# Kernel tuning notes

Measured on AMD Instinct MI355X. Metric: run time of the kernel, lower is better.

Reference implementation:

```python
import jax, jax.numpy as jnp
import numpy as np

B, C, T, D, LI = 512, 6, 77, 512, 193  # batch, noun chunks, context len, embed dim, image tokens
VOCAB = 49408


def setup_inputs() -> dict:
    key = jax.random.key(0)
    k1, k2, k3, k4 = jax.random.split(key, 4)
    return {
        "image_features": jax.random.normal(k1, (B, LI, D), dtype=jnp.float32),
        "text_features": jax.random.normal(k2, (B, T, D), dtype=jnp.float32),
        "logit_scale": jnp.ones((1,), dtype=jnp.float32) * 4.6052,
        "captions": jax.random.randint(k3, (B, T), 0, VOCAB, dtype=jnp.int32),
        "noun_chunk_mask": jax.random.randint(k4, (B, C, T), 0, 2, dtype=jnp.int32),
    }


def reference(image_features, text_features, logit_scale, captions, noun_chunk_mask):
    # global image feature: CLS token
    global_image = image_features[:, 0, :]                      # (B, D)
    # global text feature: token at argmax(captions) (EOT position in CLIP)
    eot = jnp.argmax(captions, axis=-1)                         # (B,)
    global_text = text_features[jnp.arange(text_features.shape[0]), eot]  # (B, D)
    # local text features: per-noun-chunk masked mean over the 77 token positions.
    # Original: (repeat_cap * mask).mean(dim=2) == (mask @ text_features) / 77.
    m = noun_chunk_mask.astype(text_features.dtype)             # (B, C, T) 0/1
    local_text = jnp.einsum('bct,btd->bcd', m, text_features) / float(T)  # (B, C, D)
    return (global_text, global_image, local_text, logit_scale)
```

## Files before the change

### kernel.cpp

```cpp
#include <hip/hip_runtime.h>

#define BB 512
#define CC 6
#define TT 77
#define DD 512
#define LIMG 193

__global__ __launch_bounds__(512) void clip_fused(
    const float* __restrict__ img,
    const float* __restrict__ txt,
    const float* __restrict__ ls,
    const int* __restrict__ cap,
    const int* __restrict__ mask,
    float* __restrict__ out)
{
    const int b   = blockIdx.x;
    const int tid = threadIdx.x;
    const int col = tid & 127;
    const int q   = tid >> 7;

    __shared__ float m[CC * TT];
    __shared__ int   wred[8];
    __shared__ float4 part[4][CC][128];

    const int* mrow = mask + (size_t)b * (CC * TT);
    for (int i = tid; i < CC * TT; i += 512) m[i] = (float)mrow[i];

    const int* crow = cap + (size_t)b * TT;
    int key = -1;
    if (tid < TT) key = (crow[tid] << 8) | (255 - tid);
    #pragma unroll
    for (int off = 32; off; off >>= 1) key = max(key, __shfl_down(key, off));
    if ((tid & 63) == 0) wred[tid >> 6] = key;
    __syncthreads();

    int kmax = wred[0];
    #pragma unroll
    for (int w = 1; w < 8; w++) kmax = max(kmax, wred[w]);
    const int eot = 255 - (kmax & 255);

    const float4* trow = (const float4*)(txt + (size_t)b * (TT * DD));

    if (q == 0) {
        float4 g = trow[(size_t)eot * 128 + col];
        ((float4*)out)[(size_t)b * 128 + col] = g;
    } else if (q == 1) {
        const float4* irow = (const float4*)(img + (size_t)b * (LIMG * DD));
        ((float4*)(out + (size_t)BB * DD))[(size_t)b * 128 + col] = irow[col];
    }

    float4 acc[CC];
    #pragma unroll
    for (int c = 0; c < CC; c++) acc[c] = make_float4(0.f, 0.f, 0.f, 0.f);

    #pragma unroll 5
    for (int t = q; t < TT; t += 4) {
        float4 v = trow[(size_t)t * 128 + col];
        #pragma unroll
        for (int c = 0; c < CC; c++) {
            float w = m[c * TT + t];
            acc[c].x += w * v.x;
            acc[c].y += w * v.y;
            acc[c].z += w * v.z;
            acc[c].w += w * v.w;
        }
    }
    #pragma unroll
    for (int c = 0; c < CC; c++) part[q][c][col] = acc[c];
    __syncthreads();

    float4* out_lt = (float4*)(out + 2 * (size_t)BB * DD);
    const float inv = 1.0f / (float)TT;
    for (int i = tid; i < CC * 128; i += 512) {
        int c  = i >> 7;
        int cc = i & 127;
        float4 s0 = part[0][c][cc];
        float4 s1 = part[1][c][cc];
        float4 s2 = part[2][c][cc];
        float4 s3 = part[3][c][cc];
        float4 r;
        r.x = (s0.x + s1.x + s2.x + s3.x) * inv;
        r.y = (s0.y + s1.y + s2.y + s3.y) * inv;
        r.z = (s0.z + s1.z + s2.z + s3.z) * inv;
        r.w = (s0.w + s1.w + s2.w + s3.w) * inv;
        out_lt[((size_t)b * CC + c) * 128 + cc] = r;
    }

    if (b == 0 && tid == 0)
        out[(size_t)2 * BB * DD + (size_t)BB * CC * DD] = ls[0];
}

extern "C" void kernel_launch(void* const* d_in, const int* in_sizes, int n_in,
                              void* d_out, int out_size, void* d_ws, size_t ws_size,
                              hipStream_t stream) {
    const float* img  = (const float*)d_in[0];
    const float* txt  = (const float*)d_in[1];
    const float* ls   = (const float*)d_in[2];
    const int*   cap  = (const int*)d_in[3];
    const int*   mask = (const int*)d_in[4];
    float* out = (float*)d_out;

    clip_fused<<<dim3(BB), dim3(512), 0, stream>>>(img, txt, ls, cap, mask, out);
}
```

Measured before the change: 286.6 us.

## Split each batch across two blocks and reduce partial sums with wave shuffles

Launches two blocks per batch, each covering half of the feature columns. Within a block, 8 lanes each take a strided subset of token positions, and their partial sums are combined with shuffle-down instead of a shared-memory partial buffer plus a second barrier. The mask is stored transposed and padded to 8 so one vector load fetches all chunk weights for a token, and launch bounds request higher occupancy. The trade-off is that adjacent lanes now read different token rows, which breaks per-row coalescing into 8-element groups, and the mask is loaded twice per batch.

```diff
diff --git a/kernel.cpp b/kernel.cpp
--- a/kernel.cpp
+++ b/kernel.cpp
@@ -6,7 +6,7 @@
 #define DD 512
 #define LIMG 193
 
-__global__ __launch_bounds__(512) void clip_fused(
+__global__ __launch_bounds__(512, 8) void clip_fused(
     const float* __restrict__ img,
     const float* __restrict__ txt,
     const float* __restrict__ ls,
@@ -14,79 +14,95 @@
     const int* __restrict__ mask,
     float* __restrict__ out)
 {
-    const int b   = blockIdx.x;
-    const int tid = threadIdx.x;
-    const int col = tid & 127;
-    const int q   = tid >> 7;
+    const int bid  = blockIdx.x;
+    const int b    = bid >> 1;
+    const int half = bid & 1;
+    const int tid  = threadIdx.x;
+    const int q    = tid & 7;
+    const int colL = tid >> 3;
+    const int col  = (half << 6) + colL;
 
-    __shared__ float m[CC * TT];
-    __shared__ int   wred[8];
-    __shared__ float4 part[4][CC][128];
+    __shared__ float mT[TT * 8];
+    __shared__ int   wred[2];
 
     const int* mrow = mask + (size_t)b * (CC * TT);
-    for (int i = tid; i < CC * TT; i += 512) m[i] = (float)mrow[i];
+    for (int i = tid; i < TT * 8; i += 512) {
+        const int c = i & 7;
+        const int t = i >> 3;
+        mT[i] = (c < CC) ? (float)mrow[c * TT + t] : 0.0f;
+    }
 
-    const int* crow = cap + (size_t)b * TT;
-    int key = -1;
-    if (tid < TT) key = (crow[tid] << 8) | (255 - tid);
-    #pragma unroll
-    for (int off = 32; off; off >>= 1) key = max(key, __shfl_down(key, off));
-    if ((tid & 63) == 0) wred[tid >> 6] = key;
+    if (half == 0) {
+        const int* crow = cap + (size_t)b * TT;
+        int key = -1;
+        if (tid < TT) key = (crow[tid] << 8) | (255 - tid);
+        if (tid < 128) {
+            #pragma unroll
+            for (int off = 32; off; off >>= 1) key = max(key, __shfl_down(key, off));
+            if ((tid & 63) == 0) wred[tid >> 6] = key;
+        }
+    }
     __syncthreads();
-
-    int kmax = wred[0];
-    #pragma unroll
-    for (int w = 1; w < 8; w++) kmax = max(kmax, wred[w]);
-    const int eot = 255 - (kmax & 255);
 
     const float4* trow = (const float4*)(txt + (size_t)b * (TT * DD));
 
-    if (q == 0) {
-        float4 g = trow[(size_t)eot * 128 + col];
-        ((float4*)out)[(size_t)b * 128 + col] = g;
-    } else if (q == 1) {
-        const float4* irow = (const float4*)(img + (size_t)b * (LIMG * DD));
-        ((float4*)(out + (size_t)BB * DD))[(size_t)b * 128 + col] = irow[col];
+    if (half == 0) {
+        if (tid < 128) {
+            const int eot = 255 - (max(wred[0], wred[1]) & 255);
+            ((float4*)out)[(size_t)b * 128 + tid] = trow[(size_t)eot * 128 + tid];
+        }
+    } else {
+        if (tid < 128) {
+            const float4* irow = (const float4*)(img + (size_t)b * (LIMG * DD));
+            ((float4*)(out + (size_t)BB * DD))[(size_t)b * 128 + tid] = irow[tid];
+        }
     }
 
     float4 acc[CC];
     #pragma unroll
     for (int c = 0; c < CC; c++) acc[c] = make_float4(0.f, 0.f, 0.f, 0.f);
 
-    #pragma unroll 5
-    for (int t = q; t < TT; t += 4) {
-        float4 v = trow[(size_t)t * 128 + col];
+    #pragma unroll 2
+    for (int t = q; t < TT; t += 8) {
+        const float4 v   = trow[(size_t)t * 128 + col];
+        const float4 m03 = *(const float4*)&mT[t * 8];
+        const float2 m45 = *(const float2*)&mT[t * 8 + 4];
+        const float mw[CC] = { m03.x, m03.y, m03.z, m03.w, m45.x, m45.y };
         #pragma unroll
         for (int c = 0; c < CC; c++) {
-            float w = m[c * TT + t];
-            acc[c].x += w * v.x;
-            acc[c].y += w * v.y;
-            acc[c].z += w * v.z;
-            acc[c].w += w * v.w;
+            acc[c].x += mw[c] * v.x;
+            acc[c].y += mw[c] * v.y;
+            acc[c].z += mw[c] * v.z;
+            acc[c].w += mw[c] * v.w;
         }
     }
+
     #pragma unroll
-    for (int c = 0; c < CC; c++) part[q][c][col] = acc[c];
-    __syncthreads();
-
-    float4* out_lt = (float4*)(out + 2 * (size_t)BB * DD);
-    const float inv = 1.0f / (float)TT;
-    for (int i = tid; i < CC * 128; i += 512) {
-        int c  = i >> 7;
-        int cc = i & 127;
-        float4 s0 = part[0][c][cc];
-        float4 s1 = part[1][c][cc];
-        float4 s2 = part[2][c][cc];
-        float4 s3 = part[3][c][cc];
-        float4 r;
-        r.x = (s0.x + s1.x + s2.x + s3.x) * inv;
-        r.y = (s0.y + s1.y + s2.y + s3.y) * inv;
-        r.z = (s0.z + s1.z + s2.z + s3.z) * inv;
-        r.w = (s0.w + s1.w + s2.w + s3.w) * inv;
-        out_lt[((size_t)b * CC + c) * 128 + cc] = r;
+    for (int off = 4; off; off >>= 1) {
+        #pragma unroll
+        for (int c = 0; c < CC; c++) {
+            acc[c].x += __shfl_down(acc[c].x, off);
+            acc[c].y += __shfl_down(acc[c].y, off);
+            acc[c].z += __shfl_down(acc[c].z, off);
+            acc[c].w += __shfl_down(acc[c].w, off);
+        }
     }
 
-    if (b == 0 && tid == 0)
+    if (q == 0) {
+        float4* out_lt = (float4*)(out + 2 * (size_t)BB * DD);
+        const float inv = 1.0f / (float)TT;
+        #pragma unroll
+        for (int c = 0; c < CC; c++) {
+            float4 r;
+            r.x = acc[c].x * inv;
+            r.y = acc[c].y * inv;
+            r.z = acc[c].z * inv;
+            r.w = acc[c].w * inv;
+            out_lt[((size_t)b * CC + c) * 128 + col] = r;
+        }
+    }
+
+    if (bid == 0 && tid == 0)
         out[(size_t)2 * BB * DD + (size_t)BB * CC * DD] = ls[0];
 }
 
@@ -100,5 +116,5 @@
     const int*   mask = (const int*)d_in[4];
     float* out = (float*)d_out;
 
-    clip_fused<<<dim3(BB), dim3(512), 0, stream>>>(img, txt, ls, cap, mask, out);
+    clip_fused<<<dim3(2 * BB), dim3(512), 0, stream>>>(img, txt, ls, cap, mask, out);
 }
```

Result: no change. 285.7 us (-0.3%).
